# Optimization experiments

Hardware: AMD Instinct MI355X
Metric: run time of the kernel (lower is better)

The kernel has to match this reference:

```python
import jax, jax.numpy as jnp
import numpy as np

EPS = 1e-8  # F.cosine_similarity default eps


def setup_inputs() -> dict:
    key = jax.random.key(0)
    k1, k2, k3, k4 = jax.random.split(key, 4)
    N, M, D, BERT_DIM = 8192, 8192, 128, 768
    return {
        "vision_feature": jax.random.normal(k1, (N, D), dtype=jnp.float32),
        "text_pooled": jax.random.normal(k2, (M, BERT_DIM), dtype=jnp.float32),
        "proj_w": jax.random.normal(k3, (D, BERT_DIM), dtype=jnp.float32) * 0.02,
        "proj_b": jax.random.normal(k4, (D,), dtype=jnp.float32) * 0.02,
    }


def reference(vision_feature, text_pooled, proj_w, proj_b):
    # proj(text_pooled): [M, 768] @ [768, D] + [D] -> [M, D]
    text_feature = text_pooled @ proj_w.T + proj_b
    # Fused cosine similarity: L2-normalize rows (with eps clamp as in
    # F.cosine_similarity), then a single [N,D]x[D,M] GEMM instead of the
    # broadcasted O(N*M*D) intermediate.
    v_norm = jnp.maximum(jnp.linalg.norm(vision_feature, axis=1, keepdims=True), EPS)
    t_norm = jnp.maximum(jnp.linalg.norm(text_feature, axis=1, keepdims=True), EPS)
    vn = vision_feature / v_norm  # [N, D]
    tn = text_feature / t_norm    # [M, D]
    similarity = vn @ tn.T        # [N, M]
    return similarity
```

## Files before the change

kernel.cpp:

```cpp
#include <hip/hip_runtime.h>
#include <stdint.h>

#define NV 8192
#define MT 8192
#define DD 128
#define KB 768

typedef __attribute__((ext_vector_type(8))) short short8;
typedef __attribute__((ext_vector_type(4))) float f32x4;

__device__ __forceinline__ ushort f2bf(float f) {
  uint32_t u = __float_as_uint(f);
  u += 0x7FFF + ((u >> 16) & 1);
  return (ushort)(u >> 16);
}

__global__ __launch_bounds__(256) void k_visnorm(const float* __restrict__ vis,
                                                 ushort* __restrict__ vn) {
  const int tx = threadIdx.x & 15;
  const int r  = blockIdx.x * 16 + (threadIdx.x >> 4);
  const float* p = vis + (size_t)r * DD + tx * 8;
  float4 a = *(const float4*)p;
  float4 b = *(const float4*)(p + 4);
  float s = a.x*a.x + a.y*a.y + a.z*a.z + a.w*a.w
          + b.x*b.x + b.y*b.y + b.z*b.z + b.w*b.w;
  s += __shfl_xor(s, 1, 16);
  s += __shfl_xor(s, 2, 16);
  s += __shfl_xor(s, 4, 16);
  s += __shfl_xor(s, 8, 16);
  const float inv = 1.0f / fmaxf(sqrtf(s), 1e-8f);
  union { ushort u[8]; uint4 v; } o;
  o.u[0] = f2bf(a.x * inv); o.u[1] = f2bf(a.y * inv);
  o.u[2] = f2bf(a.z * inv); o.u[3] = f2bf(a.w * inv);
  o.u[4] = f2bf(b.x * inv); o.u[5] = f2bf(b.y * inv);
  o.u[6] = f2bf(b.z * inv); o.u[7] = f2bf(b.w * inv);
  *(uint4*)(vn + (size_t)r * DD + tx * 8) = o.v;
}

__global__ __launch_bounds__(512) void k_proj(const float* __restrict__ txt,
                                              const float* __restrict__ w,
                                              const float* __restrict__ bias,
                                              ushort* __restrict__ tn) {
  __shared__ float wT[64][132];
  __shared__ float tt[32][68];
  const int tid = threadIdx.x;
  const int tx = tid & 15;
  const int ty = tid >> 4;
  const int rb = blockIdx.x * 32;
  const int row = rb + ty;
  const int d0 = tx * 8;

  float acc[8] = {0.f, 0.f, 0.f, 0.f, 0.f, 0.f, 0.f, 0.f};

  for (int k0 = 0; k0 < KB; k0 += 64) {
#pragma unroll
    for (int i = 0; i < 4; ++i) {
      int li = tid + i * 512;
      int d  = li >> 4;
      int k4 = (li & 15) << 2;
      float4 v = *(const float4*)(w + (size_t)d * KB + k0 + k4);
      wT[k4 + 0][d] = v.x;
      wT[k4 + 1][d] = v.y;
      wT[k4 + 2][d] = v.z;
      wT[k4 + 3][d] = v.w;
    }
    {
      int r  = tid >> 4;
      int k4 = (tid & 15) << 2;
      *(float4*)&tt[r][k4] = *(const float4*)(txt + (size_t)(rb + r) * KB + k0 + k4);
    }
    __syncthreads();

#pragma unroll 8
    for (int kk = 0; kk < 64; ++kk) {
      float t0 = tt[ty][kk];
      float4 w0 = *(const float4*)&wT[kk][d0];
      float4 w1 = *(const float4*)&wT[kk][d0 + 4];
      acc[0] = fmaf(t0, w0.x, acc[0]);
      acc[1] = fmaf(t0, w0.y, acc[1]);
      acc[2] = fmaf(t0, w0.z, acc[2]);
      acc[3] = fmaf(t0, w0.w, acc[3]);
      acc[4] = fmaf(t0, w1.x, acc[4]);
      acc[5] = fmaf(t0, w1.y, acc[5]);
      acc[6] = fmaf(t0, w1.z, acc[6]);
      acc[7] = fmaf(t0, w1.w, acc[7]);
    }
    __syncthreads();
  }

  float4 b0 = *(const float4*)(bias + d0);
  float4 b1 = *(const float4*)(bias + d0 + 4);
  acc[0] += b0.x; acc[1] += b0.y; acc[2] += b0.z; acc[3] += b0.w;
  acc[4] += b1.x; acc[5] += b1.y; acc[6] += b1.z; acc[7] += b1.w;

  float s = acc[0]*acc[0] + acc[1]*acc[1] + acc[2]*acc[2] + acc[3]*acc[3]
          + acc[4]*acc[4] + acc[5]*acc[5] + acc[6]*acc[6] + acc[7]*acc[7];
  s += __shfl_xor(s, 1, 16);
  s += __shfl_xor(s, 2, 16);
  s += __shfl_xor(s, 4, 16);
  s += __shfl_xor(s, 8, 16);
  const float inv = 1.0f / fmaxf(sqrtf(s), 1e-8f);

  union { ushort u[8]; uint4 v; } o;
#pragma unroll
  for (int i = 0; i < 8; ++i) o.u[i] = f2bf(acc[i] * inv);
  *(uint4*)(tn + (size_t)row * DD + d0) = o.v;
}

__global__ __launch_bounds__(256, 3) void k_sim(const ushort* __restrict__ vn,
                                                const ushort* __restrict__ tn,
                                                float* __restrict__ out) {
  const int lane = threadIdx.x & 63;
  const int wave = threadIdx.x >> 6;
  const int row0 = blockIdx.y * 128 + (wave >> 1) * 64;
  const int col0 = blockIdx.x * 128 + (wave & 1) * 64;
  const int lrow = lane & 15;
  const int koff = (lane >> 4) * 8;

  const ushort* ap = vn + (size_t)(row0 + lrow) * DD + koff;
  const ushort* bp = tn + (size_t)(col0 + lrow) * DD + koff;

  f32x4 acc[4][4] = {};

#pragma unroll
  for (int ks = 0; ks < 4; ++ks) {
    short8 a[4], b[4];
#pragma unroll
    for (int m = 0; m < 4; ++m)
      a[m] = *(const short8*)(ap + (size_t)m * 16 * DD + ks * 32);
#pragma unroll
    for (int n = 0; n < 4; ++n)
      b[n] = *(const short8*)(bp + (size_t)n * 16 * DD + ks * 32);
#pragma unroll
    for (int m = 0; m < 4; ++m)
#pragma unroll
      for (int n = 0; n < 4; ++n)
        acc[m][n] = __builtin_amdgcn_mfma_f32_16x16x32_bf16(a[m], b[n], acc[m][n], 0, 0, 0);
  }

  const int orow = (lane >> 4) * 4;
  const int ocol = lane & 15;
  float* op = out + (size_t)(row0 + orow) * MT + col0 + ocol;
#pragma unroll
  for (int m = 0; m < 4; ++m)
#pragma unroll
    for (int n = 0; n < 4; ++n)
#pragma unroll
      for (int j = 0; j < 4; ++j)
        op[(size_t)(m * 16 + j) * MT + n * 16] = acc[m][n][j];
}

extern "C" void kernel_launch(void* const* d_in, const int* in_sizes, int n_in,
                              void* d_out, int out_size, void* d_ws, size_t ws_size,
                              hipStream_t stream) {
  (void)in_sizes; (void)n_in; (void)out_size; (void)ws_size;
  const float* vis  = (const float*)d_in[0];
  const float* txt  = (const float*)d_in[1];
  const float* w    = (const float*)d_in[2];
  const float* bias = (const float*)d_in[3];
  float* out = (float*)d_out;

  ushort* vn = (ushort*)d_ws;
  ushort* tn = vn + (size_t)NV * DD;

  k_visnorm<<<NV / 16, 256, 0, stream>>>(vis, vn);
  k_proj<<<MT / 32, 512, 0, stream>>>(txt, w, bias, tn);
  k_sim<<<dim3(MT / 128, NV / 128), 256, 0, stream>>>(vn, tn, out);
}
```

Measured before the change: 150.6 us.

## Replace FP32 SIMT projection with bf16 MFMA GEMM plus separate norm kernel

Replaces the shared-memory FP32 FMA projection kernel with a pipeline: convert text and weights to bf16, run an MFMA-based GEMM writing fp32 projections to workspace, then a separate kernel adds bias, L2-normalizes and emits bf16. This moves the 8192x768x128 projection onto matrix cores instead of scalar FMAs. In exchange it adds extra global round trips (a bf16 copy of text, an fp32 intermediate) and two more launches, and it lowers projection precision to bf16 inputs.

Result: faster. 121.2 us (-19.6%).

```diff
diff --git a/kernel.cpp b/kernel.cpp
--- a/kernel.cpp
+++ b/kernel.cpp
@@ -37,74 +37,85 @@
   *(uint4*)(vn + (size_t)r * DD + tx * 8) = o.v;
 }
 
-__global__ __launch_bounds__(512) void k_proj(const float* __restrict__ txt,
-                                              const float* __restrict__ w,
-                                              const float* __restrict__ bias,
-                                              ushort* __restrict__ tn) {
-  __shared__ float wT[64][132];
-  __shared__ float tt[32][68];
-  const int tid = threadIdx.x;
-  const int tx = tid & 15;
-  const int ty = tid >> 4;
-  const int rb = blockIdx.x * 32;
-  const int row = rb + ty;
-  const int d0 = tx * 8;
+__global__ __launch_bounds__(256) void k_cvt(const float* __restrict__ src,
+                                             ushort* __restrict__ dst) {
+  const size_t i = ((size_t)blockIdx.x * 256 + threadIdx.x) * 8;
+  float4 a = *(const float4*)(src + i);
+  float4 b = *(const float4*)(src + i + 4);
+  union { ushort u[8]; uint4 v; } o;
+  o.u[0] = f2bf(a.x); o.u[1] = f2bf(a.y); o.u[2] = f2bf(a.z); o.u[3] = f2bf(a.w);
+  o.u[4] = f2bf(b.x); o.u[5] = f2bf(b.y); o.u[6] = f2bf(b.z); o.u[7] = f2bf(b.w);
+  *(uint4*)(dst + i) = o.v;
+}
 
-  float acc[8] = {0.f, 0.f, 0.f, 0.f, 0.f, 0.f, 0.f, 0.f};
+__global__ __launch_bounds__(64) void k_projmfma(const ushort* __restrict__ tb,
+                                                 const ushort* __restrict__ wb,
+                                                 float* __restrict__ tf) {
+  const int lane = threadIdx.x;
+  const int row0 = blockIdx.y * 64;
+  const int col0 = blockIdx.x * 64;
+  const int lrow = lane & 15;
+  const int koff = (lane >> 4) * 8;
 
-  for (int k0 = 0; k0 < KB; k0 += 64) {
+  const ushort* ap = tb + (size_t)(row0 + lrow) * KB + koff;
+  const ushort* bp = wb + (size_t)(col0 + lrow) * KB + koff;
+
+  f32x4 acc[4][4] = {};
+
+#pragma unroll 4
+  for (int ks = 0; ks < KB / 32; ++ks) {
+    short8 a[4], b[4];
 #pragma unroll
-    for (int i = 0; i < 4; ++i) {
-      int li = tid + i * 512;
-      int d  = li >> 4;
-      int k4 = (li & 15) << 2;
-      float4 v = *(const float4*)(w + (size_t)d * KB + k0 + k4);
-      wT[k4 + 0][d] = v.x;
-      wT[k4 + 1][d] = v.y;
-      wT[k4 + 2][d] = v.z;
-      wT[k4 + 3][d] = v.w;
-    }
-    {
-      int r  = tid >> 4;
-      int k4 = (tid & 15) << 2;
-      *(float4*)&tt[r][k4] = *(const float4*)(txt + (size_t)(rb + r) * KB + k0 + k4);
-    }
-    __syncthreads();
-
-#pragma unroll 8
-    for (int kk = 0; kk < 64; ++kk) {
-      float t0 = tt[ty][kk];
-      float4 w0 = *(const float4*)&wT[kk][d0];
-      float4 w1 = *(const float4*)&wT[kk][d0 + 4];
-      acc[0] = fmaf(t0, w0.x, acc[0]);
-      acc[1] = fmaf(t0, w0.y, acc[1]);
-      acc[2] = fmaf(t0, w0.z, acc[2]);
-      acc[3] = fmaf(t0, w0.w, acc[3]);
-      acc[4] = fmaf(t0, w1.x, acc[4]);
-      acc[5] = fmaf(t0, w1.y, acc[5]);
-      acc[6] = fmaf(t0, w1.z, acc[6]);
-      acc[7] = fmaf(t0, w1.w, acc[7]);
-    }
-    __syncthreads();
+    for (int m = 0; m < 4; ++m)
+      a[m] = *(const short8*)(ap + (size_t)m * 16 * KB + ks * 32);
+#pragma unroll
+    for (int n = 0; n < 4; ++n)
+      b[n] = *(const short8*)(bp + (size_t)n * 16 * KB + ks * 32);
+#pragma unroll
+    for (int m = 0; m < 4; ++m)
+#pragma unroll
+      for (int n = 0; n < 4; ++n)
+        acc[m][n] = __builtin_amdgcn_mfma_f32_16x16x32_bf16(a[m], b[n], acc[m][n], 0, 0, 0);
   }
 
-  float4 b0 = *(const float4*)(bias + d0);
-  float4 b1 = *(const float4*)(bias + d0 + 4);
-  acc[0] += b0.x; acc[1] += b0.y; acc[2] += b0.z; acc[3] += b0.w;
-  acc[4] += b1.x; acc[5] += b1.y; acc[6] += b1.z; acc[7] += b1.w;
+  const int orow = (lane >> 4) * 4;
+  const int ocol = lane & 15;
+  float* op = tf + (size_t)(row0 + orow) * DD + col0 + ocol;
+#pragma unroll
+  for (int m = 0; m < 4; ++m)
+#pragma unroll
+    for (int n = 0; n < 4; ++n)
+#pragma unroll
+      for (int j = 0; j < 4; ++j)
+        op[(size_t)(m * 16 + j) * DD + n * 16] = acc[m][n][j];
+}
 
-  float s = acc[0]*acc[0] + acc[1]*acc[1] + acc[2]*acc[2] + acc[3]*acc[3]
-          + acc[4]*acc[4] + acc[5]*acc[5] + acc[6]*acc[6] + acc[7]*acc[7];
+__global__ __launch_bounds__(256) void k_tnorm(const float* __restrict__ tf,
+                                               const float* __restrict__ bias,
+                                               ushort* __restrict__ tn) {
+  const int tx = threadIdx.x & 15;
+  const int r  = blockIdx.x * 16 + (threadIdx.x >> 4);
+  const int d0 = tx * 8;
+  const float* p = tf + (size_t)r * DD + d0;
+  float4 a = *(const float4*)p;
+  float4 b = *(const float4*)(p + 4);
+  float4 ba = *(const float4*)(bias + d0);
+  float4 bb = *(const float4*)(bias + d0 + 4);
+  a.x += ba.x; a.y += ba.y; a.z += ba.z; a.w += ba.w;
+  b.x += bb.x; b.y += bb.y; b.z += bb.z; b.w += bb.w;
+  float s = a.x*a.x + a.y*a.y + a.z*a.z + a.w*a.w
+          + b.x*b.x + b.y*b.y + b.z*b.z + b.w*b.w;
   s += __shfl_xor(s, 1, 16);
   s += __shfl_xor(s, 2, 16);
   s += __shfl_xor(s, 4, 16);
   s += __shfl_xor(s, 8, 16);
   const float inv = 1.0f / fmaxf(sqrtf(s), 1e-8f);
-
   union { ushort u[8]; uint4 v; } o;
-#pragma unroll
-  for (int i = 0; i < 8; ++i) o.u[i] = f2bf(acc[i] * inv);
-  *(uint4*)(tn + (size_t)row * DD + d0) = o.v;
+  o.u[0] = f2bf(a.x * inv); o.u[1] = f2bf(a.y * inv);
+  o.u[2] = f2bf(a.z * inv); o.u[3] = f2bf(a.w * inv);
+  o.u[4] = f2bf(b.x * inv); o.u[5] = f2bf(b.y * inv);
+  o.u[6] = f2bf(b.z * inv); o.u[7] = f2bf(b.w * inv);
+  *(uint4*)(tn + (size_t)r * DD + d0) = o.v;
 }
 
 __global__ __launch_bounds__(256, 3) void k_sim(const ushort* __restrict__ vn,
@@ -160,10 +171,17 @@
   const float* bias = (const float*)d_in[3];
   float* out = (float*)d_out;
 
-  ushort* vn = (ushort*)d_ws;
-  ushort* tn = vn + (size_t)NV * DD;
+  char* ws = (char*)d_ws;
+  ushort* vn = (ushort*)(ws);
+  ushort* tn = (ushort*)(ws + (size_t)2097152);
+  ushort* tb = (ushort*)(ws + (size_t)4194304);
+  ushort* wb = (ushort*)(ws + (size_t)16777216);
+  float*  tf = (float*) (ws + (size_t)16973824);
 
   k_visnorm<<<NV / 16, 256, 0, stream>>>(vis, vn);
-  k_proj<<<MT / 32, 512, 0, stream>>>(txt, w, bias, tn);
+  k_cvt<<<(MT * KB) / 2048, 256, 0, stream>>>(txt, tb);
+  k_cvt<<<(DD * KB) / 2048, 256, 0, stream>>>(w, wb);
+  k_projmfma<<<dim3(2, MT / 64), 64, 0, stream>>>(tb, wb, tf);
+  k_tnorm<<<MT / 16, 256, 0, stream>>>(tf, bias, tn);
   k_sim<<<dim3(MT / 128, NV / 128), 256, 0, stream>>>(vn, tn, out);
 }
```
